# Performance work log

Measured on AMD Instinct MI355X. Metric: run time of the kernel, lower is better.

The kernel has to match this reference:

```python
import jax, jax.numpy as jnp
import numpy as np

N_NODES = 10000
IN_FEAT = 16
HID = 64
TCH = 32
B, W, E = 4, 12, 320000


def setup_inputs() -> dict:
    key = jax.random.key(0)
    ks = jax.random.split(key, 12)
    x = jax.random.normal(ks[0], (B, W, N_NODES, IN_FEAT), dtype=jnp.float32)
    edge_index = jax.random.randint(ks[1], (2, E), 0, N_NODES, dtype=jnp.int32)
    s = lambda fan: 1.0 / np.sqrt(fan)
    W1 = jax.random.uniform(ks[2], (IN_FEAT, HID), jnp.float32, -s(IN_FEAT), s(IN_FEAT))
    b1 = jnp.zeros((HID,), jnp.float32)
    W2 = jax.random.uniform(ks[3], (HID, HID), jnp.float32, -s(HID), s(HID))
    b2 = jnp.zeros((HID,), jnp.float32)
    conv1_w = jax.random.uniform(ks[4], (TCH, HID, 3), jnp.float32, -s(HID * 3), s(HID * 3))
    conv1_b = jax.random.uniform(ks[5], (TCH,), jnp.float32, -s(HID * 3), s(HID * 3))
    conv2_w = jax.random.uniform(ks[6], (TCH, TCH, 3), jnp.float32, -s(TCH * 3), s(TCH * 3))
    conv2_b = jax.random.uniform(ks[7], (TCH,), jnp.float32, -s(TCH * 3), s(TCH * 3))
    fc_w = jax.random.uniform(ks[8], (1, TCH), jnp.float32, -s(TCH), s(TCH))
    fc_b = jax.random.uniform(ks[9], (1,), jnp.float32, -s(TCH), s(TCH))
    return {"x": x, "edge_index": edge_index, "W1": W1, "b1": b1, "W2": W2,
            "b2": b2, "conv1_w": conv1_w, "conv1_b": conv1_b,
            "conv2_w": conv2_w, "conv2_b": conv2_b, "fc_w": fc_w, "fc_b": fc_b}


def _conv1d(h, w, b):
    # h: (BN, C_in, W), w: (C_out, C_in, K)
    out = jax.lax.conv_general_dilated(h, w, window_strides=(1,), padding=[(1, 1)],
                                       dimension_numbers=("NCH", "OIH", "NCH"))
    return out + b[None, :, None]


def reference(x, edge_index, W1, b1, W2, b2, conv1_w, conv1_b, conv2_w, conv2_b, fc_w, fc_b):
    Bb, Ww, Nn, Ff = x.shape
    BN = Bb * Nn
    src, dst = edge_index[0], edge_index[1]
    # PyG GCNConv norm with self-loops over ALL BN nodes (edges touch only first N)
    deg = jnp.zeros((BN,), x.dtype).at[dst].add(1.0) + 1.0  # in-degree + self-loop
    dinv = jax.lax.rsqrt(deg)
    norm_e = dinv[src] * dinv[dst]          # (E,)
    self_norm = dinv * dinv                 # 1/deg, self-loop weight

    def gcn(h, Wm, bm):
        m = h @ Wm                           # (BN, out)
        agg = jnp.zeros_like(m).at[dst].add(norm_e[:, None] * m[src])
        return agg + self_norm[:, None] * m + bm

    xt = x.transpose(1, 0, 2, 3).reshape(Ww, BN, Ff)  # (W, BN, F), node idx = b*N+n

    def step(h):
        h = jax.nn.relu(gcn(h, W1, b1))
        h = jax.nn.relu(gcn(h, W2, b2))
        return h

    H = jax.vmap(step)(xt)                   # (W, BN, HID)
    H = H.transpose(1, 2, 0)                 # (BN, HID, W)
    H = jax.nn.relu(_conv1d(H, conv1_w, conv1_b))
    H = jax.nn.relu(_conv1d(H, conv2_w, conv2_b))
    H_last = H[:, :, -1]                     # (BN, TCH)
    out = H_last @ fc_w.T + fc_b             # (BN, 1)
    return out.reshape(Bb, Nn)
```

## Files before the change

### kernel.cpp

```cpp
#include <hip/hip_runtime.h>

#define N_NODES 10000
#define BN_TOT  40000
#define HID     64
#define IN_F    16
#define TCH     32
#define NW      12
#define RSTRIDE 192

__global__ void hist_kernel(const int* __restrict__ dst, int* __restrict__ cnt, int E) {
    int e = blockIdx.x * blockDim.x + threadIdx.x;
    if (e < E) atomicAdd(&cnt[dst[e]], 1);
}

__global__ __launch_bounds__(1024) void scan_kernel(const int* __restrict__ cnt,
                                                    int* __restrict__ row_ptr,
                                                    int* __restrict__ fill_pos,
                                                    float* __restrict__ dinv) {
    __shared__ int part[1024];
    int t = threadIdx.x;
    int base = t * 10;
    int s = 0;
#pragma unroll
    for (int k = 0; k < 10; ++k) {
        int b = base + k;
        if (b < N_NODES) s += cnt[b];
    }
    part[t] = s;
    __syncthreads();
    for (int off = 1; off < 1024; off <<= 1) {
        int v = 0;
        if (t >= off) v = part[t - off];
        __syncthreads();
        part[t] += v;
        __syncthreads();
    }
    int running = (t == 0) ? 0 : part[t - 1];
#pragma unroll
    for (int k = 0; k < 10; ++k) {
        int b = base + k;
        if (b < N_NODES) {
            row_ptr[b]  = running;
            fill_pos[b] = running;
            int c = cnt[b];
            dinv[b] = rsqrtf((float)c + 1.0f);
            running += c;
        }
    }
    if (t == 1023) row_ptr[N_NODES] = part[1023];
}

__global__ void fill_kernel(const int* __restrict__ src, const int* __restrict__ dst,
                            const float* __restrict__ dinv,
                            int* __restrict__ fill_pos,
                            int2* __restrict__ edges, int E) {
    int e = blockIdx.x * blockDim.x + threadIdx.x;
    if (e >= E) return;
    int s = src[e], d = dst[e];
    int pos = atomicAdd(&fill_pos[d], 1);
    edges[pos] = make_int2(s * (RSTRIDE * 4), __float_as_int(dinv[s] * dinv[d]));
}

__global__ void prep_kernel(const float* __restrict__ c1w, const float* __restrict__ c2w,
                            float4* __restrict__ w1p, float2* __restrict__ w2p) {
    int idx = blockIdx.x * blockDim.x + threadIdx.x;
    if (idx < 2048) {
        int tc = idx & 31, ic = idx >> 5;
        const float* p = c1w + tc * 192 + ic * 3;
        w1p[idx] = make_float4(p[0], p[1], p[2], 0.f);
    } else {
        int i2 = idx - 2048;
        int tc = i2 & 31, ic = i2 >> 5;
        const float* p = c2w + tc * 96 + ic * 3;
        w2p[i2] = make_float2(p[0], p[1]);
    }
}

__global__ __launch_bounds__(256) void gemm1_kernel(const float* __restrict__ x,
                                                    const float* __restrict__ W1,
                                                    float* __restrict__ m) {
    int idx = blockIdx.x * blockDim.x + threadIdx.x;
    int oc = idx & 63;
    int n = __builtin_amdgcn_readfirstlane(idx >> 6);
    const float* xb = x + (size_t)n * IN_F;
    float s0 = 0.f, s1 = 0.f, s2 = 0.f;
#pragma unroll
    for (int f = 0; f < IN_F; ++f) {
        float wv = W1[f * HID + oc];
        s0 += xb[(size_t)9  * N_NODES * IN_F + f] * wv;
        s1 += xb[(size_t)10 * N_NODES * IN_F + f] * wv;
        s2 += xb[(size_t)11 * N_NODES * IN_F + f] * wv;
    }
    float* mr = m + (size_t)n * RSTRIDE;
    mr[oc] = s0; mr[64 + oc] = s1; mr[128 + oc] = s2;
}

__global__ __launch_bounds__(256, 8) void gatherA_kernel(
        const float* __restrict__ m, const int* __restrict__ row_ptr,
        const int2* __restrict__ edges,
        const float* __restrict__ dinv, const float* __restrict__ b1,
        const float* __restrict__ W2, float* __restrict__ m2) {
    __shared__ float hs[4][3][HID];
    int gid = blockIdx.x * blockDim.x + threadIdx.x;
    int lane = threadIdx.x & 63;
    int wv = threadIdx.x >> 6;
    int row = __builtin_amdgcn_readfirstlane(gid >> 6);
    const int lo0 = lane * 4, lo1 = 256 + lane * 4, lo2 = 512 + lane * 4;
    const char* mrow = (const char*)m + (size_t)row * (RSTRIDE * 4);
    float dv = dinv[row];
    float sn = dv * dv;
    float s0 = sn * *(const float*)(mrow + lo0);
    float s1 = sn * *(const float*)(mrow + lo1);
    float s2 = sn * *(const float*)(mrow + lo2);
    int j = row_ptr[row], end = row_ptr[row + 1];
    for (; j + 3 < end; j += 4) {
        int2 e0 = edges[j], e1 = edges[j + 1], e2 = edges[j + 2], e3 = edges[j + 3];
        const char* q0 = (const char*)m + e0.x;
        const char* q1 = (const char*)m + e1.x;
        const char* q2 = (const char*)m + e2.x;
        const char* q3 = (const char*)m + e3.x;
        float w0 = __int_as_float(e0.y), w1 = __int_as_float(e1.y);
        float w2 = __int_as_float(e2.y), w3 = __int_as_float(e3.y);
        s0 += w0 * *(const float*)(q0 + lo0) + w1 * *(const float*)(q1 + lo0)
            + w2 * *(const float*)(q2 + lo0) + w3 * *(const float*)(q3 + lo0);
        s1 += w0 * *(const float*)(q0 + lo1) + w1 * *(const float*)(q1 + lo1)
            + w2 * *(const float*)(q2 + lo1) + w3 * *(const float*)(q3 + lo1);
        s2 += w0 * *(const float*)(q0 + lo2) + w1 * *(const float*)(q1 + lo2)
            + w2 * *(const float*)(q2 + lo2) + w3 * *(const float*)(q3 + lo2);
    }
    for (; j < end; ++j) {
        int2 e = edges[j];
        const char* q = (const char*)m + e.x;
        float w = __int_as_float(e.y);
        s0 += w * *(const float*)(q + lo0);
        s1 += w * *(const float*)(q + lo1);
        s2 += w * *(const float*)(q + lo2);
    }
    float bb = b1[lane];
    hs[wv][0][lane] = fmaxf(s0 + bb, 0.f);
    hs[wv][1][lane] = fmaxf(s1 + bb, 0.f);
    hs[wv][2][lane] = fmaxf(s2 + bb, 0.f);
    __builtin_amdgcn_wave_barrier();
    const float4* h0v = (const float4*)&hs[wv][0][0];
    const float4* h1v = (const float4*)&hs[wv][1][0];
    const float4* h2v = (const float4*)&hs[wv][2][0];
    float t0 = 0.f, t1 = 0.f, t2 = 0.f;
#pragma unroll
    for (int ic4 = 0; ic4 < 16; ++ic4) {
        float4 h0 = h0v[ic4], h1 = h1v[ic4], h2 = h2v[ic4];
        float wA = W2[(ic4 * 4 + 0) * HID + lane];
        float wB = W2[(ic4 * 4 + 1) * HID + lane];
        float wC = W2[(ic4 * 4 + 2) * HID + lane];
        float wD = W2[(ic4 * 4 + 3) * HID + lane];
        t0 += h0.x * wA + h0.y * wB + h0.z * wC + h0.w * wD;
        t1 += h1.x * wA + h1.y * wB + h1.z * wC + h1.w * wD;
        t2 += h2.x * wA + h2.y * wB + h2.z * wC + h2.w * wD;
    }
    float* m2r = m2 + (size_t)row * RSTRIDE;
    m2r[lane] = t0; m2r[64 + lane] = t1; m2r[128 + lane] = t2;
}

__global__ __launch_bounds__(512, 6) void convfc_kernel(
        const float* __restrict__ mB, const int* __restrict__ row_ptr,
        const int2* __restrict__ edges,
        const float* __restrict__ dinv, const float* __restrict__ b2,
        const float* __restrict__ x, const float* __restrict__ W1,
        const float* __restrict__ b1, const float* __restrict__ W2,
        const float4* __restrict__ w1p, const float* __restrict__ b1c,
        const float2* __restrict__ w2p, const float* __restrict__ b2c,
        const float* __restrict__ fcw, const float* __restrict__ fcb,
        float* __restrict__ out) {
    __shared__ float2 w1s01[2048];
    __shared__ float  w1s2[2048];
    __shared__ float  sm[8][768];
    int t = threadIdx.x;
#pragma unroll
    for (int i = 0; i < 4; ++i) {
        float4 wv4 = w1p[i * 512 + t];
        w1s01[i * 512 + t] = make_float2(wv4.x, wv4.y);
        w1s2[i * 512 + t] = wv4.z;
    }
    __syncthreads();

    int wv = t >> 6, lane = t & 63;
    int w = __builtin_amdgcn_readfirstlane(blockIdx.x * 8 + wv);
    float* hsw = sm[wv];

    {
        const int lo0 = lane * 4, lo1 = 256 + lane * 4, lo2 = 512 + lane * 4;
        const char* mrow = (const char*)mB + (size_t)w * (RSTRIDE * 4);
        float dv = dinv[w];
        float sn = dv * dv;
        float s0 = sn * *(const float*)(mrow + lo0);
        float s1 = sn * *(const float*)(mrow + lo1);
        float s2 = sn * *(const float*)(mrow + lo2);
        int j = row_ptr[w], end = row_ptr[w + 1];
        for (; j + 3 < end; j += 4) {
            int2 e0 = edges[j], e1 = edges[j + 1], e2 = edges[j + 2], e3 = edges[j + 3];
            const char* q0 = (const char*)mB + e0.x;
            const char* q1 = (const char*)mB + e1.x;
            const char* q2 = (const char*)mB + e2.x;
            const char* q3 = (const char*)mB + e3.x;
            float w0 = __int_as_float(e0.y), w1 = __int_as_float(e1.y);
            float w2 = __int_as_float(e2.y), w3 = __int_as_float(e3.y);
            s0 += w0 * *(const float*)(q0 + lo0) + w1 * *(const float*)(q1 + lo0)
                + w2 * *(const float*)(q2 + lo0) + w3 * *(const float*)(q3 + lo0);
            s1 += w0 * *(const float*)(q0 + lo1) + w1 * *(const float*)(q1 + lo1)
                + w2 * *(const float*)(q2 + lo1) + w3 * *(const float*)(q3 + lo1);
            s2 += w0 * *(const float*)(q0 + lo2) + w1 * *(const float*)(q1 + lo2)
                + w2 * *(const float*)(q2 + lo2) + w3 * *(const float*)(q3 + lo2);
        }
        for (; j < end; ++j) {
            int2 e = edges[j];
            const char* q = (const char*)mB + e.x;
            float ww = __int_as_float(e.y);
            s0 += ww * *(const float*)(q + lo0);
            s1 += ww * *(const float*)(q + lo1);
            s2 += ww * *(const float*)(q + lo2);
        }
        float bb = b2[lane];
        hsw[0 * 192 + 0 * 64 + lane] = fmaxf(s0 + bb, 0.f);
        hsw[0 * 192 + 1 * 64 + lane] = fmaxf(s1 + bb, 0.f);
        hsw[0 * 192 + 2 * 64 + lane] = fmaxf(s2 + bb, 0.f);
    }

    {
        float w1r[16];
#pragma unroll
        for (int f = 0; f < IN_F; ++f) w1r[f] = W1[f * HID + lane];
        float s[9];
#pragma unroll
        for (int k = 1; k <= 3; ++k) {
#pragma unroll
            for (int tt = 0; tt < 3; ++tt) {
                const float* xp = x + ((size_t)(k * NW + 9 + tt) * N_NODES + w) * IN_F;
                float a = 0.f;
#pragma unroll
                for (int f = 0; f < IN_F; ++f) a += xp[f] * w1r[f];
                s[(k - 1) * 3 + tt] = a;
            }
        }
        float bb1 = b1[lane];
#pragma unroll
        for (int k = 1; k <= 3; ++k) {
            hsw[k * 192 + 0 * 64 + lane] = fmaxf(s[(k - 1) * 3 + 0] + bb1, 0.f);
            hsw[k * 192 + 1 * 64 + lane] = fmaxf(s[(k - 1) * 3 + 1] + bb1, 0.f);
            hsw[k * 192 + 2 * 64 + lane] = fmaxf(s[(k - 1) * 3 + 2] + bb1, 0.f);
        }
        __builtin_amdgcn_wave_barrier();
        float acc[9];
#pragma unroll
        for (int mm = 0; mm < 9; ++mm) acc[mm] = 0.f;
#pragma unroll
        for (int k4 = 0; k4 < 16; ++k4) {
            float wA = W2[(k4 * 4 + 0) * HID + lane];
            float wB = W2[(k4 * 4 + 1) * HID + lane];
            float wC = W2[(k4 * 4 + 2) * HID + lane];
            float wD = W2[(k4 * 4 + 3) * HID + lane];
#pragma unroll
            for (int k = 1; k <= 3; ++k) {
#pragma unroll
                for (int tt = 0; tt < 3; ++tt) {
                    float4 h = ((const float4*)&hsw[k * 192 + tt * 64])[k4];
                    acc[(k - 1) * 3 + tt] += h.x * wA + h.y * wB + h.z * wC + h.w * wD;
                }
            }
        }
        __builtin_amdgcn_wave_barrier();
        float bb2 = b2[lane];
#pragma unroll
        for (int k = 1; k <= 3; ++k) {
            hsw[k * 192 + 0 * 64 + lane] = fmaxf(acc[(k - 1) * 3 + 0] + bb2, 0.f);
            hsw[k * 192 + 1 * 64 + lane] = fmaxf(acc[(k - 1) * 3 + 1] + bb2, 0.f);
            hsw[k * 192 + 2 * 64 + lane] = fmaxf(acc[(k - 1) * 3 + 2] + bb2, 0.f);
        }
    }
    __builtin_amdgcn_wave_barrier();

    int pos = lane >> 5, tc = lane & 31;
    int pA = pos, pB = pos + 1, pC = (pos == 0) ? 2 : 0;
    float hCs = (pos == 0) ? 1.f : 0.f;
    float a1[4];
    float bc1 = b1c[tc];
#pragma unroll
    for (int r = 0; r < 4; ++r) a1[r] = bc1;
#pragma unroll
    for (int ic4 = 0; ic4 < 16; ++ic4) {
        float2 wa01 = w1s01[(ic4 * 4 + 0) * 32 + tc];
        float2 wb01 = w1s01[(ic4 * 4 + 1) * 32 + tc];
        float2 wc01 = w1s01[(ic4 * 4 + 2) * 32 + tc];
        float2 wd01 = w1s01[(ic4 * 4 + 3) * 32 + tc];
        float waz = w1s2[(ic4 * 4 + 0) * 32 + tc] * hCs;
        float wbz = w1s2[(ic4 * 4 + 1) * 32 + tc] * hCs;
        float wcz = w1s2[(ic4 * 4 + 2) * 32 + tc] * hCs;
        float wdz = w1s2[(ic4 * 4 + 3) * 32 + tc] * hCs;
#pragma unroll
        for (int r = 0; r < 4; ++r) {
            float4 hA = ((const float4*)&hsw[r * 192 + pA * 64])[ic4];
            float4 hB = ((const float4*)&hsw[r * 192 + pB * 64])[ic4];
            float4 hC = ((const float4*)&hsw[r * 192 + pC * 64])[ic4];
            a1[r] += hA.x * wa01.x + hB.x * wa01.y + hC.x * waz
                   + hA.y * wb01.x + hB.y * wb01.y + hC.y * wbz
                   + hA.z * wc01.x + hB.z * wc01.y + hC.z * wcz
                   + hA.w * wd01.x + hB.w * wd01.y + hC.w * wdz;
        }
    }
    __builtin_amdgcn_wave_barrier();
#pragma unroll
    for (int r = 0; r < 4; ++r) hsw[r * 64 + pos * 32 + tc] = fmaxf(a1[r], 0.f);
    __builtin_amdgcn_wave_barrier();

    int rr = pos * 2;
    float bc2 = b2c[tc];
    float a2q0 = bc2, a2q1 = bc2;
#pragma unroll
    for (int ic4 = 0; ic4 < 8; ++ic4) {
        float2 w0 = w2p[(ic4 * 4 + 0) * 32 + tc];
        float2 w1 = w2p[(ic4 * 4 + 1) * 32 + tc];
        float2 w2v = w2p[(ic4 * 4 + 2) * 32 + tc];
        float2 w3 = w2p[(ic4 * 4 + 3) * 32 + tc];
        float4 cA0 = ((const float4*)&hsw[(rr + 0) * 64 + 0])[ic4];
        float4 cB0 = ((const float4*)&hsw[(rr + 0) * 64 + 32])[ic4];
        float4 cA1 = ((const float4*)&hsw[(rr + 1) * 64 + 0])[ic4];
        float4 cB1 = ((const float4*)&hsw[(rr + 1) * 64 + 32])[ic4];
        a2q0 += cA0.x * w0.x + cB0.x * w0.y + cA0.y * w1.x + cB0.y * w1.y
              + cA0.z * w2v.x + cB0.z * w2v.y + cA0.w * w3.x + cB0.w * w3.y;
        a2q1 += cA1.x * w0.x + cB1.x * w0.y + cA1.y * w1.x + cB1.y * w1.y
              + cA1.z * w2v.x + cB1.z * w2v.y + cA1.w * w3.x + cB1.w * w3.y;
    }
    float fw = fcw[tc];
    float r0v = fmaxf(a2q0, 0.f) * fw;
    float r1v = fmaxf(a2q1, 0.f) * fw;
#pragma unroll
    for (int off = 16; off > 0; off >>= 1) {
        r0v += __shfl_down(r0v, off, 32);
        r1v += __shfl_down(r1v, off, 32);
    }
    if (tc == 0) {
        float fb = fcb[0];
        out[w + (rr + 0) * N_NODES] = r0v + fb;
        out[w + (rr + 1) * N_NODES] = r1v + fb;
    }
}

extern "C" void kernel_launch(void* const* d_in, const int* in_sizes, int n_in,
                              void* d_out, int out_size, void* d_ws, size_t ws_size,
                              hipStream_t stream) {
    const float* x   = (const float*)d_in[0];
    const int*   ei  = (const int*)d_in[1];
    const float* W1  = (const float*)d_in[2];
    const float* b1  = (const float*)d_in[3];
    const float* W2  = (const float*)d_in[4];
    const float* b2  = (const float*)d_in[5];
    const float* c1w = (const float*)d_in[6];
    const float* c1b = (const float*)d_in[7];
    const float* c2w = (const float*)d_in[8];
    const float* c2b = (const float*)d_in[9];
    const float* fcw = (const float*)d_in[10];
    const float* fcb = (const float*)d_in[11];
    float* out = (float*)d_out;

    const int E = in_sizes[1] / 2;
    const int* src = ei;
    const int* dst = ei + E;

    const size_t SG = (size_t)N_NODES * RSTRIDE;
    int*    cnt      = (int*)d_ws;
    int*    row_ptr  = cnt + 10240;
    int*    fill_pos = row_ptr + 10240;
    int2*   edges    = (int2*)(fill_pos + 10240);
    float*  dinv     = (float*)(edges + E);
    float4* w1p      = (float4*)(dinv + 10240);
    float2* w2p      = (float2*)(w1p + 2048);
    float*  mA       = (float*)(w2p + 1024);
    float*  mB       = mA + SG;

    hipMemsetAsync(cnt, 0, N_NODES * sizeof(int), stream);
    hist_kernel<<<(E + 255) / 256, 256, 0, stream>>>(dst, cnt, E);
    scan_kernel<<<1, 1024, 0, stream>>>(cnt, row_ptr, fill_pos, dinv);
    fill_kernel<<<(E + 255) / 256, 256, 0, stream>>>(src, dst, dinv, fill_pos, edges, E);
    prep_kernel<<<12, 256, 0, stream>>>(c1w, c2w, w1p, w2p);

    gemm1_kernel <<<(N_NODES * HID) / 256, 256, 0, stream>>>(x, W1, mA);
    gatherA_kernel<<<(N_NODES * HID) / 256, 256, 0, stream>>>(mA, row_ptr, edges, dinv, b1, W2, mB);

    convfc_kernel<<<N_NODES / 8, 512, 0, stream>>>(mB, row_ptr, edges, dinv, b2,
                                                   x, W1, b1, W2,
                                                   w1p, c1b, w2p, c2b, fcw, fcb, out);
}
```

Baseline: 156.9 us.

## Aggregate raw inputs before W1 projection and fuse gemm1 into gather kernel

Uses linearity of the first GCN layer to aggregate the 16-wide input features over neighbors first, then apply W1, instead of projecting to 64-wide and aggregating. This removes the gemm1 kernel and the intermediate mA buffer, and it shrinks the per-edge gather from 192 floats to 48 floats. The edge offset encoding changes to x row stride, so convfc rescales it by 12, which adds a multiply per edge. Lanes 48-63 duplicate timestep 11 work, and the gather loop is unrolled by 8.

Measured after the change: 142.8 us. 1.1x faster.

```diff
diff --git a/kernel.cpp b/kernel.cpp
--- a/kernel.cpp
+++ b/kernel.cpp
@@ -58,7 +58,7 @@
     if (e >= E) return;
     int s = src[e], d = dst[e];
     int pos = atomicAdd(&fill_pos[d], 1);
-    edges[pos] = make_int2(s * (RSTRIDE * 4), __float_as_int(dinv[s] * dinv[d]));
+    edges[pos] = make_int2(s * 64, __float_as_int(dinv[s] * dinv[d]));
 }
 
 __global__ void prep_kernel(const float* __restrict__ c1w, const float* __restrict__ c2w,
@@ -76,85 +76,77 @@
     }
 }
 
-__global__ __launch_bounds__(256) void gemm1_kernel(const float* __restrict__ x,
-                                                    const float* __restrict__ W1,
-                                                    float* __restrict__ m) {
-    int idx = blockIdx.x * blockDim.x + threadIdx.x;
-    int oc = idx & 63;
-    int n = __builtin_amdgcn_readfirstlane(idx >> 6);
-    const float* xb = x + (size_t)n * IN_F;
-    float s0 = 0.f, s1 = 0.f, s2 = 0.f;
-#pragma unroll
-    for (int f = 0; f < IN_F; ++f) {
-        float wv = W1[f * HID + oc];
-        s0 += xb[(size_t)9  * N_NODES * IN_F + f] * wv;
-        s1 += xb[(size_t)10 * N_NODES * IN_F + f] * wv;
-        s2 += xb[(size_t)11 * N_NODES * IN_F + f] * wv;
-    }
-    float* mr = m + (size_t)n * RSTRIDE;
-    mr[oc] = s0; mr[64 + oc] = s1; mr[128 + oc] = s2;
-}
-
-__global__ __launch_bounds__(256, 8) void gatherA_kernel(
-        const float* __restrict__ m, const int* __restrict__ row_ptr,
-        const int2* __restrict__ edges,
-        const float* __restrict__ dinv, const float* __restrict__ b1,
+__global__ __launch_bounds__(256, 8) void gatherX_kernel(
+        const float* __restrict__ x, const int* __restrict__ row_ptr,
+        const int2* __restrict__ edges, const float* __restrict__ dinv,
+        const float* __restrict__ W1, const float* __restrict__ b1,
         const float* __restrict__ W2, float* __restrict__ m2) {
+    __shared__ float xs[4][64];
     __shared__ float hs[4][3][HID];
     int gid = blockIdx.x * blockDim.x + threadIdx.x;
     int lane = threadIdx.x & 63;
     int wv = threadIdx.x >> 6;
     int row = __builtin_amdgcn_readfirstlane(gid >> 6);
-    const int lo0 = lane * 4, lo1 = 256 + lane * 4, lo2 = 512 + lane * 4;
-    const char* mrow = (const char*)m + (size_t)row * (RSTRIDE * 4);
+    int tt = lane >> 4; if (tt > 2) tt = 2;
+    int f = lane & 15;
+    const char* xlane = (const char*)(x + (size_t)(9 + tt) * N_NODES * IN_F + f);
     float dv = dinv[row];
-    float sn = dv * dv;
-    float s0 = sn * *(const float*)(mrow + lo0);
-    float s1 = sn * *(const float*)(mrow + lo1);
-    float s2 = sn * *(const float*)(mrow + lo2);
+    float s = dv * dv * *(const float*)(xlane + row * 64);
     int j = row_ptr[row], end = row_ptr[row + 1];
-    for (; j + 3 < end; j += 4) {
-        int2 e0 = edges[j], e1 = edges[j + 1], e2 = edges[j + 2], e3 = edges[j + 3];
-        const char* q0 = (const char*)m + e0.x;
-        const char* q1 = (const char*)m + e1.x;
-        const char* q2 = (const char*)m + e2.x;
-        const char* q3 = (const char*)m + e3.x;
-        float w0 = __int_as_float(e0.y), w1 = __int_as_float(e1.y);
-        float w2 = __int_as_float(e2.y), w3 = __int_as_float(e3.y);
-        s0 += w0 * *(const float*)(q0 + lo0) + w1 * *(const float*)(q1 + lo0)
-            + w2 * *(const float*)(q2 + lo0) + w3 * *(const float*)(q3 + lo0);
-        s1 += w0 * *(const float*)(q0 + lo1) + w1 * *(const float*)(q1 + lo1)
-            + w2 * *(const float*)(q2 + lo1) + w3 * *(const float*)(q3 + lo1);
-        s2 += w0 * *(const float*)(q0 + lo2) + w1 * *(const float*)(q1 + lo2)
-            + w2 * *(const float*)(q2 + lo2) + w3 * *(const float*)(q3 + lo2);
+    for (; j + 7 < end; j += 8) {
+        int2 e0 = edges[j],     e1 = edges[j + 1], e2 = edges[j + 2], e3 = edges[j + 3];
+        int2 e4 = edges[j + 4], e5 = edges[j + 5], e6 = edges[j + 6], e7 = edges[j + 7];
+        float v0 = *(const float*)(xlane + e0.x);
+        float v1 = *(const float*)(xlane + e1.x);
+        float v2 = *(const float*)(xlane + e2.x);
+        float v3 = *(const float*)(xlane + e3.x);
+        float v4 = *(const float*)(xlane + e4.x);
+        float v5 = *(const float*)(xlane + e5.x);
+        float v6 = *(const float*)(xlane + e6.x);
+        float v7 = *(const float*)(xlane + e7.x);
+        s += __int_as_float(e0.y) * v0 + __int_as_float(e1.y) * v1
+           + __int_as_float(e2.y) * v2 + __int_as_float(e3.y) * v3
+           + __int_as_float(e4.y) * v4 + __int_as_float(e5.y) * v5
+           + __int_as_float(e6.y) * v6 + __int_as_float(e7.y) * v7;
     }
     for (; j < end; ++j) {
         int2 e = edges[j];
-        const char* q = (const char*)m + e.x;
-        float w = __int_as_float(e.y);
-        s0 += w * *(const float*)(q + lo0);
-        s1 += w * *(const float*)(q + lo1);
-        s2 += w * *(const float*)(q + lo2);
+        s += __int_as_float(e.y) * *(const float*)(xlane + e.x);
+    }
+    xs[wv][lane] = s;
+    __builtin_amdgcn_wave_barrier();
+
+    float w1r[16];
+#pragma unroll
+    for (int ff = 0; ff < IN_F; ++ff) w1r[ff] = W1[ff * HID + lane];
+    float h0 = 0.f, h1v = 0.f, h2 = 0.f;
+#pragma unroll
+    for (int ff = 0; ff < IN_F; ++ff) {
+        float wv1 = w1r[ff];
+        h0  += wv1 * xs[wv][ff];
+        h1v += wv1 * xs[wv][16 + ff];
+        h2  += wv1 * xs[wv][32 + ff];
     }
     float bb = b1[lane];
-    hs[wv][0][lane] = fmaxf(s0 + bb, 0.f);
-    hs[wv][1][lane] = fmaxf(s1 + bb, 0.f);
-    hs[wv][2][lane] = fmaxf(s2 + bb, 0.f);
-    __builtin_amdgcn_wave_barrier();
-    const float4* h0v = (const float4*)&hs[wv][0][0];
-    const float4* h1v = (const float4*)&hs[wv][1][0];
-    const float4* h2v = (const float4*)&hs[wv][2][0];
+    hs[wv][0][lane] = fmaxf(h0 + bb, 0.f);
+    hs[wv][1][lane] = fmaxf(h1v + bb, 0.f);
+    hs[wv][2][lane] = fmaxf(h2 + bb, 0.f);
+    __builtin_amdgcn_wave_barrier();
+
+    const float4* h0v4 = (const float4*)&hs[wv][0][0];
+    const float4* h1v4 = (const float4*)&hs[wv][1][0];
+    const float4* h2v4 = (const float4*)&hs[wv][2][0];
     float t0 = 0.f, t1 = 0.f, t2 = 0.f;
 #pragma unroll
     for (int ic4 = 0; ic4 < 16; ++ic4) {
-        float4 h0 = h0v[ic4], h1 = h1v[ic4], h2 = h2v[ic4];
+        float4 a0 = h0v4[ic4], a1 = h1v4[ic4], a2 = h2v4[ic4];
         float wA = W2[(ic4 * 4 + 0) * HID + lane];
         float wB = W2[(ic4 * 4 + 1) * HID + lane];
         float wC = W2[(ic4 * 4 + 2) * HID + lane];
         float wD = W2[(ic4 * 4 + 3) * HID + lane];
-        t0 += h0.x * wA + h0.y * wB + h0.z * wC + h0.w * wD;
-        t1 += h1.x * wA + h1.y * wB + h1.z * wC + h1.w * wD;
-        t2 += h2.x * wA + h2.y * wB + h2.z * wC + h2.w * wD;
+        t0 += a0.x * wA + a0.y * wB + a0.z * wC + a0.w * wD;
+        t1 += a1.x * wA + a1.y * wB + a1.z * wC + a1.w * wD;
+        t2 += a2.x * wA + a2.y * wB + a2.z * wC + a2.w * wD;
     }
     float* m2r = m2 + (size_t)row * RSTRIDE;
     m2r[lane] = t0; m2r[64 + lane] = t1; m2r[128 + lane] = t2;
@@ -197,10 +189,10 @@
         int j = row_ptr[w], end = row_ptr[w + 1];
         for (; j + 3 < end; j += 4) {
             int2 e0 = edges[j], e1 = edges[j + 1], e2 = edges[j + 2], e3 = edges[j + 3];
-            const char* q0 = (const char*)mB + e0.x;
-            const char* q1 = (const char*)mB + e1.x;
-            const char* q2 = (const char*)mB + e2.x;
-            const char* q3 = (const char*)mB + e3.x;
+            const char* q0 = (const char*)mB + e0.x * 12;
+            const char* q1 = (const char*)mB + e1.x * 12;
+            const char* q2 = (const char*)mB + e2.x * 12;
+            const char* q3 = (const char*)mB + e3.x * 12;
             float w0 = __int_as_float(e0.y), w1 = __int_as_float(e1.y);
             float w2 = __int_as_float(e2.y), w3 = __int_as_float(e3.y);
             s0 += w0 * *(const float*)(q0 + lo0) + w1 * *(const float*)(q1 + lo0)
@@ -212,7 +204,7 @@
         }
         for (; j < end; ++j) {
             int2 e = edges[j];
-            const char* q = (const char*)mB + e.x;
+            const char* q = (const char*)mB + e.x * 12;
             float ww = __int_as_float(e.y);
             s0 += ww * *(const float*)(q + lo0);
             s1 += ww * *(const float*)(q + lo1);
@@ -372,8 +364,7 @@
     float*  dinv     = (float*)(edges + E);
     float4* w1p      = (float4*)(dinv + 10240);
     float2* w2p      = (float2*)(w1p + 2048);
-    float*  mA       = (float*)(w2p + 1024);
-    float*  mB       = mA + SG;
+    float*  mB       = (float*)(w2p + 1024);
 
     hipMemsetAsync(cnt, 0, N_NODES * sizeof(int), stream);
     hist_kernel<<<(E + 255) / 256, 256, 0, stream>>>(dst, cnt, E);
@@ -381,8 +372,8 @@
     fill_kernel<<<(E + 255) / 256, 256, 0, stream>>>(src, dst, dinv, fill_pos, edges, E);
     prep_kernel<<<12, 256, 0, stream>>>(c1w, c2w, w1p, w2p);
 
-    gemm1_kernel <<<(N_NODES * HID) / 256, 256, 0, stream>>>(x, W1, mA);
-    gatherA_kernel<<<(N_NODES * HID) / 256, 256, 0, stream>>>(mA, row_ptr, edges, dinv, b1, W2, mB);
+    gatherX_kernel<<<(N_NODES * HID) / 256, 256, 0, stream>>>(x, row_ptr, edges, dinv,
+                                                              W1, b1, W2, mB);
 
     convfc_kernel<<<N_NODES / 8, 512, 0, stream>>>(mB, row_ptr, edges, dinv, b2,
                                                    x, W1, b1, W2,
```
